# Performance work log

Measured on AMD Instinct MI355X. Metric: run time of the kernel, lower is better.

The kernel has to match this reference:

```python
import jax, jax.numpy as jnp
import numpy as np
from functools import partial

B, S, T = 32, 64, 64
VS, VT = 32000, 32000
E, H = 256, 512            # embed_dim, encoder hidden per direction
DH = 2 * H                 # decoder hidden (= encoder_hidden_dim)
A = 128                    # attention_dim


def _p(key, shape, scale=0.05):
    return scale * jax.random.normal(key, shape, dtype=jnp.float32)


def setup_inputs() -> dict:
    key = jax.random.key(0)
    ks = jax.random.split(key, 32)
    inp = {
        'src': jax.random.randint(ks[0], (B, S), 0, VS),
        'tgt_input': jax.random.randint(ks[1], (B, T), 0, VT),
        # encoder
        'enc_emb': _p(ks[2], (VS, E)),
        'enc_Wih_f': _p(ks[3], (4 * H, E)), 'enc_Whh_f': _p(ks[4], (4 * H, H)),
        'enc_bih_f': _p(ks[5], (4 * H,)),  'enc_bhh_f': _p(ks[6], (4 * H,)),
        'enc_Wih_b': _p(ks[7], (4 * H, E)), 'enc_Whh_b': _p(ks[8], (4 * H, H)),
        'enc_bih_b': _p(ks[9], (4 * H,)),  'enc_bhh_b': _p(ks[10], (4 * H,)),
        # decoder
        'dec_emb': _p(ks[11], (VT, E)),
        'Wd': _p(ks[12], (A, DH)), 'bd': _p(ks[13], (A,)),
        'We': _p(ks[14], (A, DH)), 'be': _p(ks[15], (A,)),
        'v_att': _p(ks[16], (A,)), 'bv': _p(ks[17], ()),
        'dec_Wih': _p(ks[18], (4 * DH, E + DH)), 'dec_Whh': _p(ks[19], (4 * DH, DH)),
        'dec_bih': _p(ks[20], (4 * DH,)), 'dec_bhh': _p(ks[21], (4 * DH,)),
        'Wo': _p(ks[22], (VT, DH + DH)), 'bo': _p(ks[23], (VT,)),
    }
    return inp


def _lstm_cell(x, h, c, Wih, Whh, b):
    g = x @ Wih.T + h @ Whh.T + b
    i, f, gg, o = jnp.split(g, 4, axis=-1)  # PyTorch gate order: i,f,g,o
    i, f, o = jax.nn.sigmoid(i), jax.nn.sigmoid(f), jax.nn.sigmoid(o)
    c_new = f * c + i * jnp.tanh(gg)
    h_new = o * jnp.tanh(c_new)
    return h_new, c_new


def _lstm_scan(xs, Wih, Whh, b, reverse):
    # xs: [S,B,E] -> outputs [S,B,H] aligned with input positions, final (h,c)
    h0 = jnp.zeros((xs.shape[1], Whh.shape[1]), xs.dtype)
    def step(carry, x):
        h, c = carry
        h, c = _lstm_cell(x, h, c, Wih, Whh, b)
        return (h, c), h
    (hT, cT), hs = jax.lax.scan(step, (h0, h0), xs, reverse=reverse)
    return hs, hT, cT


def _forward(src, tgt_input, enc_emb,
             enc_Wih_f, enc_Whh_f, enc_bih_f, enc_bhh_f,
             enc_Wih_b, enc_Whh_b, enc_bih_b, enc_bhh_b,
             dec_emb, Wd, bd, We, be, v_att, bv,
             dec_Wih, dec_Whh, dec_bih, dec_bhh, Wo, bo):
    # ---- Encoder: bidirectional single-layer LSTM ----
    emb = enc_emb[src]                              # [B,S,E]
    xs = emb.transpose(1, 0, 2)                     # [S,B,E]
    hs_f, hT_f, cT_f = _lstm_scan(xs, enc_Wih_f, enc_Whh_f, enc_bih_f + enc_bhh_f, False)
    hs_b, hT_b, cT_b = _lstm_scan(xs, enc_Wih_b, enc_Whh_b, enc_bih_b + enc_bhh_b, True)
    enc_out = jnp.concatenate([hs_f, hs_b], axis=-1).transpose(1, 0, 2)  # [B,S,2H]
    h = jnp.concatenate([hT_f, hT_b], axis=-1)      # [B,DH]
    c = jnp.concatenate([cT_f, cT_b], axis=-1)

    # ---- Decoder with Bahdanau attention (full teacher forcing) ----
    enc_proj = enc_out @ We.T + be                  # [B,S,A] precomputed
    dec_b = dec_bih + dec_bhh
    tgt_emb = dec_emb[tgt_input].transpose(1, 0, 2)  # [T,B,E]

    def dec_step(carry, emb_t):
        h, c = carry
        dproj = h @ Wd.T + bd                       # [B,A]
        energy = jnp.tanh(dproj[:, None, :] + enc_proj)  # [B,S,A]
        scores = energy @ v_att + bv                # [B,S]
        w = jax.nn.softmax(scores, axis=1)
        ctx = jnp.einsum('bs,bsh->bh', w, enc_out)  # [B,DH]
        x = jnp.concatenate([emb_t, ctx], axis=-1)  # [B,E+DH]
        h_new, c_new = _lstm_cell(x, h, c, dec_Wih, dec_Whh, dec_b)
        logits = jnp.concatenate([h_new, ctx], axis=-1) @ Wo.T + bo  # [B,VT]
        return (h_new, c_new), logits

    _, logits = jax.lax.scan(dec_step, (h, c), tgt_emb)  # [T,B,VT]
    return logits.transpose(1, 0, 2)                     # [B,T,VT]


def reference(src, tgt_input, enc_emb,
              enc_Wih_f, enc_Whh_f, enc_bih_f, enc_bhh_f,
              enc_Wih_b, enc_Whh_b, enc_bih_b, enc_bhh_b,
              dec_emb, Wd, bd, We, be, v_att, bv,
              dec_Wih, dec_Whh, dec_bih, dec_bhh, Wo, bo):
    return _forward(src, tgt_input, enc_emb,
                    enc_Wih_f, enc_Whh_f, enc_bih_f, enc_bhh_f,
                    enc_Wih_b, enc_Whh_b, enc_bih_b, enc_bhh_b,
                    dec_emb, Wd, bd, We, be, v_att, bv,
                    dec_Wih, dec_Whh, dec_bih, dec_bhh, Wo, bo)
```

## Files before the change

### kernel.cpp

```cpp
#include <hip/hip_runtime.h>


using u16 = unsigned short;
using u32 = unsigned int;
using u64 = unsigned long long;
using f32x4 = __attribute__((ext_vector_type(4))) float;
using s16x8 = __attribute__((ext_vector_type(8))) short;
using u16x4 = __attribute__((ext_vector_type(4))) unsigned short;

__device__ __forceinline__ float sigm_(float x) { return 1.0f / (1.0f + expf(-x)); }
__device__ __forceinline__ float tanh_(float x) {
    float e = __expf(fminf(2.0f * x, 30.0f));
    return (e - 1.0f) / (e + 1.0f);
}

__device__ __forceinline__ u16 f2bf(float x) {
    u32 u = __float_as_uint(x);
    u += 0x7fffu + ((u >> 16) & 1u);
    return (u16)(u >> 16);
}
__device__ __forceinline__ u32 pk2(float a, float b) {
    return (u32)f2bf(a) | ((u32)f2bf(b) << 16);
}
__device__ __forceinline__ float bf2f(u16 v) {
    return __uint_as_float((u32)v << 16);
}

__device__ __forceinline__ void ast32(u32* p, u32 v) {
    __hip_atomic_store(p, v, __ATOMIC_RELAXED, __HIP_MEMORY_SCOPE_AGENT);
}

#define MFMA __builtin_amdgcn_mfma_f32_16x16x32_bf16

#define GLL(g, l) __builtin_amdgcn_global_load_lds( \
    (__attribute__((address_space(1))) void*)(g),   \
    (__attribute__((address_space(3))) void*)(l), 16, 0, 0)

__device__ __forceinline__ void gbar(int* cnt, int target) {
    asm volatile("s_waitcnt vmcnt(0) lgkmcnt(0)" ::: "memory");
    __syncthreads();
    if (threadIdx.x == 0) {
        __hip_atomic_fetch_add(cnt, 1, __ATOMIC_RELAXED, __HIP_MEMORY_SCOPE_AGENT);
        while (__hip_atomic_load(cnt, __ATOMIC_RELAXED, __HIP_MEMORY_SCOPE_AGENT) < target)
            __builtin_amdgcn_s_sleep(1);
    }
    __syncthreads();
}

__global__ __launch_bounds__(256) void k_zero(float* __restrict__ p, int n) {
    int i = blockIdx.x * 256 + threadIdx.x;
    if (i < n) p[i] = 0.0f;
}

__global__ __launch_bounds__(256) void k_cast_bf16(const float* __restrict__ in,
                                                   u16* __restrict__ outp, int n8) {
    int idx = blockIdx.x * 256 + threadIdx.x;
    if (idx >= n8) return;
    const f32x4* p = (const f32x4*)in + (size_t)idx * 2;
    f32x4 a = p[0], c = p[1];
    u32* o = (u32*)(outp + (size_t)idx * 8);
    o[0] = pk2(a.x, a.y); o[1] = pk2(a.z, a.w);
    o[2] = pk2(c.x, c.y); o[3] = pk2(c.z, c.w);
}

__global__ __launch_bounds__(256) void k_embed_bf(const int* __restrict__ tok,
                                                  const float* __restrict__ emb,
                                                  u16* __restrict__ outp) {
    int idx = blockIdx.x * 256 + threadIdx.x;
    int r = idx >> 6, e4 = idx & 63;
    int outer = r >> 5, b = r & 31;
    int tk = tok[b * 64 + outer];
    f32x4 v = ((const f32x4*)emb)[(size_t)tk * 64 + e4];
    u32* o = (u32*)(outp + (size_t)r * 256 + (e4 << 2));
    o[0] = pk2(v.x, v.y); o[1] = pk2(v.z, v.w);
}

__global__ __launch_bounds__(256) void k_prep_perm(
    const float* __restrict__ src, u16* __restrict__ dst,
    int J, int K4, int srcStride, int srcOff, int total)
{
    int idx = blockIdx.x * 256 + threadIdx.x;
    if (idx >= total) return;
    int n = idx / K4, kq = (idx - n * K4) << 2;
    int orig = (n & 3) * J + (n >> 2);
    f32x4 v = *(const f32x4*)(src + (size_t)orig * srcStride + srcOff + kq);
    u32* o = (u32*)(dst + (size_t)n * (K4 << 2) + kq);
    o[0] = pk2(v.x, v.y); o[1] = pk2(v.z, v.w);
}

__global__ __launch_bounds__(256) void k_prep_ws(
    const float* __restrict__ W, u16* __restrict__ dst)
{
    int idx = blockIdx.x * 256 + threadIdx.x;
    int n = idx >> 8, kp = idx & 255, k0 = kp << 1;
    int orig = (n & 3) * 512 + (n >> 2);
    const float* s = W + (size_t)orig * 512 + k0;
    int g = n >> 5, r = n & 31;
    int byteoff = (k0 << 1) ^ ((r & 7) << 4);
    *(u32*)((char*)dst + (size_t)g * 32768 + r * 1024 + byteoff) = pk2(s[0], s[1]);
}

__global__ __launch_bounds__(256) void k_prep_w2s(
    const float* __restrict__ Whh, const float* __restrict__ Wih, u16* __restrict__ dst)
{
    int idx = blockIdx.x * 256 + threadIdx.x;
    int n = idx >> 10, kp = idx & 1023, k0 = kp << 1;
    int orig = (n & 3) * 1024 + (n >> 2);
    const float* s = (k0 < 1024) ? (Whh + (size_t)orig * 1024 + k0)
                                 : (Wih + (size_t)orig * 1280 + 256 + (k0 - 1024));
    int g = n >> 5, r = n & 31;
    int byteoff = (k0 << 1) ^ ((r & 7) << 4);
    *(u32*)((char*)dst + (size_t)g * 131072 + r * 4096 + byteoff) = pk2(s[0], s[1]);
}

__global__ __launch_bounds__(256) void k_gemm_bf(
    const u16* __restrict__ A, const u16* __restrict__ B, int K,
    const float* __restrict__ b1, const float* __restrict__ b2, int biasJ,
    float* __restrict__ C, int ldc, int nM, int nN, int remapOut, int swz)
{
    __shared__ __align__(16) u16 As[128 * 32];
    __shared__ __align__(16) u16 Bs[128 * 32];
    int w = blockIdx.x;
    if (swz) { int cpx = (nM * nN) >> 3; w = (w & 7) * cpx + (w >> 3); }
    int bm = (w % nM) * 128, bn = (w / nM) * 128;
    int tid = threadIdx.x, wave = tid >> 6, lane = tid & 63;
    int wm = wave & 1, wn = wave >> 1;
    f32x4 acc[4][4] = {};

    int rA = wave * 32 + (lane >> 2);
    int cb2 = (lane & 3) * 16;
    const char* gA = (const char*)A + ((size_t)(bm + rA) * K) * 2 + cb2;
    const char* gB = (const char*)B + ((size_t)(bn + rA) * K) * 2 + cb2;
    size_t rowskip = (size_t)16 * K * 2;
    char* lA = (char*)As + wave * 2048;
    char* lB = (char*)Bs + wave * 2048;
    const u16* rdA = As + (wm * 64 + (lane & 15)) * 32 + (lane >> 4) * 8;
    const u16* rdB = Bs + (wn * 64 + (lane & 15)) * 32 + (lane >> 4) * 8;

    for (int k0 = 0; k0 < K; k0 += 32) {
        size_t kb = (size_t)k0 * 2;
        GLL(gA + kb, lA); GLL(gA + kb + rowskip, lA + 1024);
        GLL(gB + kb, lB); GLL(gB + kb + rowskip, lB + 1024);
        __syncthreads();
        s16x8 af[4], bfv[4];
#pragma unroll
        for (int m2 = 0; m2 < 4; ++m2) af[m2] = *(const s16x8*)(rdA + m2 * 512);
#pragma unroll
        for (int n2 = 0; n2 < 4; ++n2) bfv[n2] = *(const s16x8*)(rdB + n2 * 512);
#pragma unroll
        for (int m2 = 0; m2 < 4; ++m2)
#pragma unroll
            for (int n2 = 0; n2 < 4; ++n2)
                acc[m2][n2] = MFMA(af[m2], bfv[n2], acc[m2][n2], 0, 0, 0);
        __syncthreads();
    }

    int rbase = bm + wm * 64 + ((lane >> 4) << 2);
    int cbase = bn + wn * 64 + (lane & 15);
#pragma unroll
    for (int n2 = 0; n2 < 4; ++n2) {
        int col = cbase + n2 * 16;
        int bcol = biasJ ? ((col & 3) * biasJ + (col >> 2)) : col;
        float bias = (b1 ? b1[bcol] : 0.0f) + (b2 ? b2[bcol] : 0.0f);
#pragma unroll
        for (int m2 = 0; m2 < 4; ++m2) {
            f32x4 v = acc[m2][n2];
#pragma unroll
            for (int jj = 0; jj < 4; ++jj) {
                int row = rbase + m2 * 16 + jj;
                int orow = remapOut ? ((row & 31) * 64 + (row >> 5)) : row;
                C[(size_t)orow * ldc + col] = v[jj] + bias;
            }
        }
    }
}

__global__ __launch_bounds__(256, 1) void k_enc_persist(
    const u16* __restrict__ Wsf, const u16* __restrict__ Wsb,
    const float* __restrict__ Gfp, const float* __restrict__ Gbp,
    u16* __restrict__ henc,
    float* __restrict__ cfb,
    u16* __restrict__ encbf,
    int* __restrict__ bar)
{
    __shared__ __align__(16) char smem[50176];
    int tid = threadIdx.x, lane = tid & 63, q = tid >> 6;
    int dir = blockIdx.x >> 6, g = blockIdx.x & 63;
    const char* wsrc = (const char*)(dir ? Wsb : Wsf) + (size_t)g * 32768;
#pragma unroll
    for (int it = 0; it < 8; ++it)
        GLL(wsrc + it * 4096 + tid * 16, smem + it * 4096 + tid * 16);
    __syncthreads();

    float* sacc = (float*)(smem + 32768);
    u16* hst = (u16*)(smem + 49664);
    const float* Gp = dir ? Gbp : Gfp;
    float* cB = cfb + dir * 16384;
    int lr = lane & 15, lk = (lane >> 4) << 3;
    int bb = tid & 31, jl = tid >> 5;
    int n0 = g * 32, j = g * 8 + jl;
    int bi = 0;

    for (int s = 0; s < 64; ++s) {
        const u16* hA = henc + (size_t)s * 32768 + dir * 16384;
        s16x8 afr[8];
#pragma unroll
        for (int it = 0; it < 4; ++it) {
            int ke = q * 128 + it * 32 + lk;
            afr[2 * it]     = *(const s16x8*)(hA + lr * 512 + ke);
            afr[2 * it + 1] = *(const s16x8*)(hA + (lr + 16) * 512 + ke);
        }
        f32x4 acc00 = {}, acc01 = {}, acc10 = {}, acc11 = {};
#pragma unroll
        for (int it = 0; it < 4; ++it) {
            int ke = q * 128 + it * 32 + lk;
            int kb = ke << 1;
            s16x8 b0 = *(const s16x8*)(smem + lr * 1024 + (kb ^ ((lr & 7) << 4)));
            int r1 = lr + 16;
            s16x8 b1 = *(const s16x8*)(smem + r1 * 1024 + (kb ^ ((r1 & 7) << 4)));
            acc00 = MFMA(afr[2 * it], b0, acc00, 0, 0, 0);
            acc01 = MFMA(afr[2 * it], b1, acc01, 0, 0, 0);
            acc10 = MFMA(afr[2 * it + 1], b0, acc10, 0, 0, 0);
            acc11 = MFMA(afr[2 * it + 1], b1, acc11, 0, 0, 0);
        }
        int rw = (lane >> 4) << 2;
#pragma unroll
        for (int rr = 0; rr < 4; ++rr) {
            sacc[q * 1056 + (rw + rr) * 33 + lr]        = acc00[rr];
            sacc[q * 1056 + (rw + rr) * 33 + 16 + lr]   = acc01[rr];
            sacc[q * 1056 + (16 + rw + rr) * 33 + lr]      = acc10[rr];
            sacc[q * 1056 + (16 + rw + rr) * 33 + 16 + lr] = acc11[rr];
        }
        __syncthreads();
        {
            int t = dir ? (63 - s) : s;
            int c4 = jl << 2;
            float gi = 0, gf = 0, gg = 0, go2 = 0;
#pragma unroll
            for (int q2 = 0; q2 < 4; ++q2) {
                const float* sp = sacc + q2 * 1056 + bb * 33 + c4;
                gi += sp[0]; gf += sp[1]; gg += sp[2]; go2 += sp[3];
            }
            f32x4 p4 = *(const f32x4*)(Gp + ((size_t)(t * 32 + bb)) * 2048 + n0 + c4);
            gi += p4.x; gf += p4.y; gg += p4.z; go2 += p4.w;
            float* cp = cB + bb * 512 + j;
            float cn = sigm_(gf) * cp[0] + sigm_(gi) * tanhf(gg);
            cp[0] = cn;
            float h = sigm_(go2) * tanhf(cn);
            u16 h16 = f2bf(h);
            encbf[((size_t)(bb * 64 + t)) * 1024 + dir * 512 + j] = h16;
            hst[bb * 8 + jl] = h16;
        }
        __syncthreads();
        if (tid < 128) {
            int bb2 = tid >> 2, p2 = tid & 3;
            u32 wv = (u32)hst[bb2 * 8 + 2 * p2] | ((u32)hst[bb2 * 8 + 2 * p2 + 1] << 16);
            ast32((u32*)(henc + (size_t)(s + 1) * 32768 + dir * 16384) + bb2 * 256 + g * 4 + p2, wv);
        }
        gbar(bar, (++bi) * 128);
    }
}

__global__ __launch_bounds__(256) void k_dec_init(
    const u16* __restrict__ henc, const float* __restrict__ cfb,
    u16* __restrict__ hcarr, float* __restrict__ cd)
{
    int idx = blockIdx.x * 256 + threadIdx.x;
    int b = idx >> 10, j = idx & 1023;
    int dir = (j >> 9), jj = j & 511;
    hcarr[b * 2048 + j] = henc[(size_t)64 * 32768 + dir * 16384 + b * 512 + jj];
    cd[b * 1024 + j] = cfb[dir * 16384 + b * 512 + jj];
}

__global__ __launch_bounds__(256, 1) void k_dec_persist(
    const u16* __restrict__ W2s, const u16* __restrict__ encbf,
    const float* __restrict__ Prep,
    const u16* __restrict__ Wd_bf, const float* __restrict__ bd,
    const float* __restrict__ eproj, const float* __restrict__ v_att,
    const float* __restrict__ bv,
    u16* __restrict__ hcarr, float* __restrict__ cd, u16* __restrict__ Abf,
    int* __restrict__ bar)
{
    __shared__ __align__(16) char smem[148480];
    int blk = blockIdx.x, tid = threadIdx.x, lane = tid & 63, q = tid >> 6;
    bool isgate = blk < 128;
    {
        const char* src = isgate ? ((const char*)W2s + (size_t)blk * 131072)
                                 : ((const char*)encbf + (size_t)(blk - 128) * 131072);
#pragma unroll
        for (int it = 0; it < 32; ++it)
            GLL(src + it * 4096 + tid * 16, smem + it * 4096 + tid * 16);
    }
    __syncthreads();

    float* sacc = (float*)(smem + 131072);
    u16* hst    = (u16*)(smem + 147968);
    float* hsh  = (float*)(smem + 131072);
    float* red  = (float*)(smem + 135168);
    float* dp   = (float*)(smem + 136192);
    float* sc   = (float*)(smem + 136704);

    int lr = lane & 15, lk = (lane >> 4) << 3;
    int bb = tid & 31, jl = tid >> 5;
    int n0 = blk * 32, j = blk * 8 + jl;
    int b = blk - 128;
    int bi = 0;

    for (int t = 0; t < 64; ++t) {
        const u16* hcT = hcarr + (size_t)t * 65536;
        f32x4 acc00 = {}, acc01 = {}, acc10 = {}, acc11 = {};
        f32x4 p4;
        if (isgate) {
            p4 = *(const f32x4*)(Prep + ((size_t)(t * 32 + bb)) * 4096 + n0 + (jl << 2));
            s16x8 afr[16];
#pragma unroll
            for (int it = 0; it < 8; ++it) {
                int ke = q * 256 + it * 32 + lk;
                afr[2 * it]     = *(const s16x8*)(hcT + lr * 2048 + ke);
                afr[2 * it + 1] = *(const s16x8*)(hcT + (lr + 16) * 2048 + ke);
            }
#pragma unroll
            for (int it = 0; it < 8; ++it) {
                int ke = q * 256 + it * 32 + lk;
                int kb = ke << 1;
                s16x8 b0 = *(const s16x8*)(smem + lr * 4096 + (kb ^ ((lr & 7) << 4)));
                int r1 = lr + 16;
                s16x8 b1 = *(const s16x8*)(smem + r1 * 4096 + (kb ^ ((r1 & 7) << 4)));
                acc00 = MFMA(afr[2 * it], b0, acc00, 0, 0, 0);
                acc01 = MFMA(afr[2 * it], b1, acc01, 0, 0, 0);
                acc10 = MFMA(afr[2 * it + 1], b0, acc10, 0, 0, 0);
                acc11 = MFMA(afr[2 * it + 1], b1, acc11, 0, 0, 0);
            }
        } else {
            {
                u16x4 hv = *(const u16x4*)(hcT + b * 2048 + (tid << 2));
                hsh[(tid << 2) + 0] = bf2f(hv.x);
                hsh[(tid << 2) + 1] = bf2f(hv.y);
                hsh[(tid << 2) + 2] = bf2f(hv.z);
                hsh[(tid << 2) + 3] = bf2f(hv.w);
            }
            __syncthreads();
            {
                int a = tid & 127, half = tid >> 7;
                const u16* wr = Wd_bf + ((size_t)a << 10) + (half << 9);
                const float* hh = hsh + (half << 9);
                float s0 = 0, s1 = 0, s2 = 0, s3 = 0;
#pragma unroll 4
                for (int k = 0; k < 512; k += 32) {
                    s16x8 w0 = *(const s16x8*)(wr + k);
                    s16x8 w1 = *(const s16x8*)(wr + k + 8);
                    s16x8 w2 = *(const s16x8*)(wr + k + 16);
                    s16x8 w3 = *(const s16x8*)(wr + k + 24);
#pragma unroll
                    for (int e = 0; e < 8; ++e) {
                        s0 += bf2f((u16)w0[e]) * hh[k + e];
                        s1 += bf2f((u16)w1[e]) * hh[k + 8 + e];
                        s2 += bf2f((u16)w2[e]) * hh[k + 16 + e];
                        s3 += bf2f((u16)w3[e]) * hh[k + 24 + e];
                    }
                }
                red[tid] = (s0 + s1) + (s2 + s3);
            }
            __syncthreads();
            if (tid < 128) dp[tid] = red[tid] + red[tid + 128] + bd[tid];
            __syncthreads();
            {
                int si = tid >> 2, qq = tid & 3;
                const float* ep = eproj + ((size_t)(b * 64 + si)) * 128 + qq * 32;
                float s = 0.0f;
#pragma unroll 8
                for (int a2 = 0; a2 < 32; ++a2)
                    s += v_att[qq * 32 + a2] * tanh_(dp[qq * 32 + a2] + ep[a2]);
                red[tid] = s;
            }
            __syncthreads();
            if (tid < 64) {
                float x = red[tid * 4] + red[tid * 4 + 1] + red[tid * 4 + 2] + red[tid * 4 + 3] + bv[0];
                float mx = x;
#pragma unroll
                for (int off = 32; off; off >>= 1) mx = fmaxf(mx, __shfl_xor(mx, off));
                float e = __expf(x - mx), ss = e;
#pragma unroll
                for (int off = 32; off; off >>= 1) ss += __shfl_xor(ss, off);
                sc[tid] = e / ss;
            }
            __syncthreads();
            {
                const u16* eL = (const u16*)smem;
                int c0i = tid << 2;
                float c0 = 0, c1 = 0, c2 = 0, c3 = 0;
                for (int s2 = 0; s2 < 64; ++s2) {
                    float wgt = sc[s2];
                    u16x4 rp = *(const u16x4*)(eL + s2 * 1024 + c0i);
                    c0 += wgt * bf2f(rp.x); c1 += wgt * bf2f(rp.y);
                    c2 += wgt * bf2f(rp.z); c3 += wgt * bf2f(rp.w);
                }
                u32 w0 = pk2(c0, c1), w1 = pk2(c2, c3);
                u32* hw = (u32*)hcT + b * 1024 + 512 + (tid << 1);
                ast32(hw, w0); ast32(hw + 1, w1);
                u32* aw = (u32*)(Abf + ((size_t)(t * 32 + b)) * 2048 + 1024 + c0i);
                aw[0] = w0; aw[1] = w1;
            }
        }
        gbar(bar, (++bi) * 160);
        if (isgate) {
            s16x8 afr[16];
#pragma unroll
            for (int it = 0; it < 8; ++it) {
                int ke = 1024 + q * 256 + it * 32 + lk;
                afr[2 * it]     = *(const s16x8*)(hcT + lr * 2048 + ke);
                afr[2 * it + 1] = *(const s16x8*)(hcT + (lr + 16) * 2048 + ke);
            }
#pragma unroll
            for (int it = 0; it < 8; ++it) {
                int ke = 1024 + q * 256 + it * 32 + lk;
                int kb = ke << 1;
                s16x8 b0 = *(const s16x8*)(smem + lr * 4096 + (kb ^ ((lr & 7) << 4)));
                int r1 = lr + 16;
                s16x8 b1 = *(const s16x8*)(smem + r1 * 4096 + (kb ^ ((r1 & 7) << 4)));
                acc00 = MFMA(afr[2 * it], b0, acc00, 0, 0, 0);
                acc01 = MFMA(afr[2 * it], b1, acc01, 0, 0, 0);
                acc10 = MFMA(afr[2 * it + 1], b0, acc10, 0, 0, 0);
                acc11 = MFMA(afr[2 * it + 1], b1, acc11, 0, 0, 0);
            }
            int rw = (lane >> 4) << 2;
#pragma unroll
            for (int rr = 0; rr < 4; ++rr) {
                sacc[q * 1056 + (rw + rr) * 33 + lr]        = acc00[rr];
                sacc[q * 1056 + (rw + rr) * 33 + 16 + lr]   = acc01[rr];
                sacc[q * 1056 + (16 + rw + rr) * 33 + lr]      = acc10[rr];
                sacc[q * 1056 + (16 + rw + rr) * 33 + 16 + lr] = acc11[rr];
            }
            __syncthreads();
            {
                int c4 = jl << 2;
                float gi = 0, gf = 0, gg = 0, go2 = 0;
#pragma unroll
                for (int q2 = 0; q2 < 4; ++q2) {
                    const float* sp = sacc + q2 * 1056 + bb * 33 + c4;
                    gi += sp[0]; gf += sp[1]; gg += sp[2]; go2 += sp[3];
                }
                gi += p4.x; gf += p4.y; gg += p4.z; go2 += p4.w;
                int ci = bb * 1024 + j;
                float cn = sigm_(gf) * cd[ci] + sigm_(gi) * tanhf(gg);
                cd[ci] = cn;
                float h = sigm_(go2) * tanhf(cn);
                u16 h16 = f2bf(h);
                Abf[((size_t)(t * 32 + bb)) * 2048 + j] = h16;
                hst[bb * 8 + jl] = h16;
            }
            __syncthreads();
            if (tid < 128) {
                int bb2 = tid >> 2, p2 = tid & 3;
                u32 wv = (u32)hst[bb2 * 8 + 2 * p2] | ((u32)hst[bb2 * 8 + 2 * p2 + 1] << 16);
                ast32((u32*)(hcarr + (size_t)(t + 1) * 65536) + bb2 * 1024 + blk * 4 + p2, wv);
            }
        }
        gbar(bar, (++bi) * 160);
    }
}

extern "C" void kernel_launch(void* const* d_in, const int* in_sizes, int n_in,
                              void* d_out, int out_size, void* d_ws, size_t ws_size,
                              hipStream_t stream)
{
    (void)in_sizes; (void)n_in; (void)out_size; (void)ws_size;
    const int*   src     = (const int*)d_in[0];
    const int*   tgt     = (const int*)d_in[1];
    const float* enc_emb = (const float*)d_in[2];
    const float* eWih_f  = (const float*)d_in[3];
    const float* eWhh_f  = (const float*)d_in[4];
    const float* ebih_f  = (const float*)d_in[5];
    const float* ebhh_f  = (const float*)d_in[6];
    const float* eWih_b  = (const float*)d_in[7];
    const float* eWhh_b  = (const float*)d_in[8];
    const float* ebih_b  = (const float*)d_in[9];
    const float* ebhh_b  = (const float*)d_in[10];
    const float* dec_emb = (const float*)d_in[11];
    const float* Wd      = (const float*)d_in[12];
    const float* bd      = (const float*)d_in[13];
    const float* We      = (const float*)d_in[14];
    const float* be      = (const float*)d_in[15];
    const float* v_att   = (const float*)d_in[16];
    const float* bv      = (const float*)d_in[17];
    const float* dWih    = (const float*)d_in[18];
    const float* dWhh    = (const float*)d_in[19];
    const float* dbih    = (const float*)d_in[20];
    const float* dbhh    = (const float*)d_in[21];
    const float* Wo      = (const float*)d_in[22];
    const float* bo      = (const float*)d_in[23];
    float* out = (float*)d_out;

    char* wp = (char*)d_ws;
    auto alloc = [&](size_t nbytes) -> void* {
        void* p = (void*)wp;
        wp += (nbytes + 255) & ~(size_t)255;
        return p;
    };
    u16*   Xe_bf = (u16*)alloc(2048u * 256 * 2);
    u16*   Ed_bf = (u16*)alloc(2048u * 256 * 2);
    float* Gf_p  = (float*)alloc(2048u * 2048 * 4);
    float* Gb_p  = (float*)alloc(2048u * 2048 * 4);
    float* Pre_p = (float*)alloc(2048u * 4096 * 4);
    float* zr    = (float*)alloc(131584u);
    float* cfb   = zr;
    int*   cnts  = (int*)((char*)zr + 131072);
    u16*   henc  = (u16*)alloc(65u * 32768 * 2);
    u16*   hcarr = (u16*)alloc(65u * 65536 * 2);
    u16*   encbf = (u16*)alloc(2048u * 1024 * 2);
    float* eproj = (float*)alloc(2048u * 128 * 4);
    float* cd    = (float*)alloc(32768u * 4);
    u16*   Abf   = (u16*)alloc(2048u * 2048 * 2);
    u16*   Wbf   = (u16*)alloc(32000u * 2048 * 2);
    u16*   W2s   = (u16*)alloc(4096u * 2048 * 2);
    u16*   Wsf   = (u16*)alloc(2048u * 512 * 2);
    u16*   Wsb   = (u16*)alloc(2048u * 512 * 2);
    u16*   Wembf = (u16*)alloc(2048u * 256 * 2);
    u16*   Wembb = (u16*)alloc(2048u * 256 * 2);
    u16*   Wembd = (u16*)alloc(4096u * 256 * 2);
    u16*   We_bf = (u16*)alloc(128u * 1024 * 2);
    u16*   Wd_bf = (u16*)alloc(128u * 1024 * 2);

    k_zero<<<129, 256, 0, stream>>>(zr, 32896);
    k_zero<<<64, 256, 0, stream>>>((float*)henc, 16384);

    k_cast_bf16<<<32000, 256, 0, stream>>>(Wo, Wbf, 8192000);
    k_cast_bf16<<<64, 256, 0, stream>>>(We, We_bf, 16384);
    k_cast_bf16<<<64, 256, 0, stream>>>(Wd, Wd_bf, 16384);
    k_prep_perm<<<512, 256, 0, stream>>>(eWih_f, Wembf, 512, 64, 256, 0, 131072);
    k_prep_perm<<<512, 256, 0, stream>>>(eWih_b, Wembb, 512, 64, 256, 0, 131072);
    k_prep_perm<<<1024, 256, 0, stream>>>(dWih, Wembd, 1024, 64, 1280, 0, 262144);
    k_prep_ws<<<2048, 256, 0, stream>>>(eWhh_f, Wsf);
    k_prep_ws<<<2048, 256, 0, stream>>>(eWhh_b, Wsb);
    k_prep_w2s<<<16384, 256, 0, stream>>>(dWhh, dWih, W2s);

    k_embed_bf<<<512, 256, 0, stream>>>(src, enc_emb, Xe_bf);
    k_embed_bf<<<512, 256, 0, stream>>>(tgt, dec_emb, Ed_bf);

    k_gemm_bf<<<256, 256, 0, stream>>>(Xe_bf, Wembf, 256, ebih_f, ebhh_f, 512,
                                       Gf_p, 2048, 16, 16, 0, 1);
    k_gemm_bf<<<256, 256, 0, stream>>>(Xe_bf, Wembb, 256, ebih_b, ebhh_b, 512,
                                       Gb_p, 2048, 16, 16, 0, 1);
    k_gemm_bf<<<512, 256, 0, stream>>>(Ed_bf, Wembd, 256, dbih, dbhh, 1024,
                                       Pre_p, 4096, 16, 32, 0, 1);

    k_enc_persist<<<128, 256, 0, stream>>>(Wsf, Wsb, Gf_p, Gb_p, henc, cfb, encbf, cnts);

    k_gemm_bf<<<16, 256, 0, stream>>>(encbf, We_bf, 1024, be, nullptr, 0,
                                      eproj, 128, 16, 1, 0, 1);
    k_dec_init<<<128, 256, 0, stream>>>(henc, cfb, hcarr, cd);

    k_dec_persist<<<160, 256, 0, stream>>>(W2s, encbf, Pre_p, Wd_bf, bd, eproj,
                                           v_att, bv, hcarr, cd, Abf, cnts + 64);

    k_gemm_bf<<<4000, 256, 0, stream>>>(Abf, Wbf, 2048, bo, nullptr, 0,
                                        out, 32000, 16, 250, 1, 1);
}
```

Measured before the change: 2.375 ms.

## Precompute encoder-context projection and use per-step hierarchical flag barriers in decoder

```diff
diff --git a/kernel.cpp b/kernel.cpp
--- a/kernel.cpp
+++ b/kernel.cpp
@@ -36,15 +36,24 @@
     (__attribute__((address_space(1))) void*)(g),   \
     (__attribute__((address_space(3))) void*)(l), 16, 0, 0)
 
-__device__ __forceinline__ void gbar(int* cnt, int target) {
+__device__ __forceinline__ void poll8(const int* go8) {
+    if (threadIdx.x < 8) {
+        const int* p = go8 + threadIdx.x * 16;
+        while (__hip_atomic_load(p, __ATOMIC_RELAXED, __HIP_MEMORY_SCOPE_AGENT) == 0)
+            __builtin_amdgcn_s_sleep(1);
+    }
+    __syncthreads();
+    asm volatile("" ::: "memory");
+}
+__device__ __forceinline__ void arrive8(int* cnt8, int* go8, int line, int perline) {
     asm volatile("s_waitcnt vmcnt(0) lgkmcnt(0)" ::: "memory");
     __syncthreads();
     if (threadIdx.x == 0) {
-        __hip_atomic_fetch_add(cnt, 1, __ATOMIC_RELAXED, __HIP_MEMORY_SCOPE_AGENT);
-        while (__hip_atomic_load(cnt, __ATOMIC_RELAXED, __HIP_MEMORY_SCOPE_AGENT) < target)
-            __builtin_amdgcn_s_sleep(1);
-    }
-    __syncthreads();
+        int old = __hip_atomic_fetch_add(cnt8 + line * 16, 1, __ATOMIC_RELAXED,
+                                         __HIP_MEMORY_SCOPE_AGENT);
+        if (old == perline - 1)
+            __hip_atomic_store(go8 + line * 16, 1, __ATOMIC_RELAXED, __HIP_MEMORY_SCOPE_AGENT);
+    }
 }
 
 __global__ __launch_bounds__(256) void k_zero(float* __restrict__ p, int n) {
@@ -100,23 +109,23 @@
     *(u32*)((char*)dst + (size_t)g * 32768 + r * 1024 + byteoff) = pk2(s[0], s[1]);
 }
 
-__global__ __launch_bounds__(256) void k_prep_w2s(
-    const float* __restrict__ Whh, const float* __restrict__ Wih, u16* __restrict__ dst)
+__global__ __launch_bounds__(256) void k_prep_whhs(
+    const float* __restrict__ Whh, u16* __restrict__ dst)
 {
     int idx = blockIdx.x * 256 + threadIdx.x;
-    int n = idx >> 10, kp = idx & 1023, k0 = kp << 1;
+    int n = idx >> 9, kp = idx & 511, k0 = kp << 1;
     int orig = (n & 3) * 1024 + (n >> 2);
-    const float* s = (k0 < 1024) ? (Whh + (size_t)orig * 1024 + k0)
-                                 : (Wih + (size_t)orig * 1280 + 256 + (k0 - 1024));
-    int g = n >> 5, r = n & 31;
+    const float* s = Whh + (size_t)orig * 1024 + k0;
+    int g = n >> 6, r = n & 63;
     int byteoff = (k0 << 1) ^ ((r & 7) << 4);
-    *(u32*)((char*)dst + (size_t)g * 131072 + r * 4096 + byteoff) = pk2(s[0], s[1]);
+    *(u32*)((char*)dst + (size_t)g * 131072 + r * 2048 + byteoff) = pk2(s[0], s[1]);
 }
 
 __global__ __launch_bounds__(256) void k_gemm_bf(
     const u16* __restrict__ A, const u16* __restrict__ B, int K,
     const float* __restrict__ b1, const float* __restrict__ b2, int biasJ,
-    float* __restrict__ C, int ldc, int nM, int nN, int remapOut, int swz)
+    float* __restrict__ C, int ldc, int nM, int nN, int remapOut, int swz,
+    u16* __restrict__ outT)
 {
     __shared__ __align__(16) u16 As[128 * 32];
     __shared__ __align__(16) u16 Bs[128 * 32];
@@ -157,6 +166,20 @@
 
     int rbase = bm + wm * 64 + ((lane >> 4) << 2);
     int cbase = bn + wn * 64 + (lane & 15);
+    if (outT) {
+#pragma unroll
+        for (int n2 = 0; n2 < 4; ++n2) {
+            int col = cbase + n2 * 16;
+#pragma unroll
+            for (int m2 = 0; m2 < 4; ++m2) {
+                f32x4 v = acc[m2][n2];
+                int row = rbase + m2 * 16;
+                u32* o = (u32*)(outT + (size_t)col * 2048 + row);
+                o[0] = pk2(v[0], v[1]); o[1] = pk2(v[2], v[3]);
+            }
+        }
+        return;
+    }
 #pragma unroll
     for (int n2 = 0; n2 < 4; ++n2) {
         int col = cbase + n2 * 16;
@@ -181,7 +204,7 @@
     u16* __restrict__ henc,
     float* __restrict__ cfb,
     u16* __restrict__ encbf,
-    int* __restrict__ bar)
+    int* __restrict__ cnt8, int* __restrict__ go8)
 {
     __shared__ __align__(16) char smem[50176];
     int tid = threadIdx.x, lane = tid & 63, q = tid >> 6;
@@ -199,9 +222,11 @@
     int lr = lane & 15, lk = (lane >> 4) << 3;
     int bb = tid & 31, jl = tid >> 5;
     int n0 = g * 32, j = g * 8 + jl;
-    int bi = 0;
 
     for (int s = 0; s < 64; ++s) {
+        if (s) poll8(go8 + s * 128);
+        int t = dir ? (63 - s) : s;
+        f32x4 p4 = *(const f32x4*)(Gp + ((size_t)(t * 32 + bb)) * 2048 + n0 + (jl << 2));
         const u16* hA = henc + (size_t)s * 32768 + dir * 16384;
         s16x8 afr[8];
 #pragma unroll
@@ -233,7 +258,6 @@
         }
         __syncthreads();
         {
-            int t = dir ? (63 - s) : s;
             int c4 = jl << 2;
             float gi = 0, gf = 0, gg = 0, go2 = 0;
 #pragma unroll
@@ -241,7 +265,6 @@
                 const float* sp = sacc + q2 * 1056 + bb * 33 + c4;
                 gi += sp[0]; gf += sp[1]; gg += sp[2]; go2 += sp[3];
             }
-            f32x4 p4 = *(const f32x4*)(Gp + ((size_t)(t * 32 + bb)) * 2048 + n0 + c4);
             gi += p4.x; gf += p4.y; gg += p4.z; go2 += p4.w;
             float* cp = cB + bb * 512 + j;
             float cn = sigm_(gf) * cp[0] + sigm_(gi) * tanhf(gg);
@@ -257,7 +280,7 @@
             u32 wv = (u32)hst[bb2 * 8 + 2 * p2] | ((u32)hst[bb2 * 8 + 2 * p2 + 1] << 16);
             ast32((u32*)(henc + (size_t)(s + 1) * 32768 + dir * 16384) + bb2 * 256 + g * 4 + p2, wv);
         }
-        gbar(bar, (++bi) * 128);
+        arrive8(cnt8 + (s + 1) * 128, go8 + (s + 1) * 128, blockIdx.x & 7, 16);
     }
 }
 
@@ -268,25 +291,27 @@
     int idx = blockIdx.x * 256 + threadIdx.x;
     int b = idx >> 10, j = idx & 1023;
     int dir = (j >> 9), jj = j & 511;
-    hcarr[b * 2048 + j] = henc[(size_t)64 * 32768 + dir * 16384 + b * 512 + jj];
+    hcarr[b * 1024 + j] = henc[(size_t)64 * 32768 + dir * 16384 + b * 512 + jj];
     cd[b * 1024 + j] = cfb[dir * 16384 + b * 512 + jj];
 }
 
 __global__ __launch_bounds__(256, 1) void k_dec_persist(
-    const u16* __restrict__ W2s, const u16* __restrict__ encbf,
-    const float* __restrict__ Prep,
+    const u16* __restrict__ Whhs, const u16* __restrict__ encbf,
+    const float* __restrict__ Prep, const u16* __restrict__ ectxT,
     const u16* __restrict__ Wd_bf, const float* __restrict__ bd,
     const float* __restrict__ eproj, const float* __restrict__ v_att,
     const float* __restrict__ bv,
     u16* __restrict__ hcarr, float* __restrict__ cd, u16* __restrict__ Abf,
-    int* __restrict__ bar)
-{
-    __shared__ __align__(16) char smem[148480];
-    int blk = blockIdx.x, tid = threadIdx.x, lane = tid & 63, q = tid >> 6;
-    bool isgate = blk < 128;
+    float* __restrict__ wbuf,
+    int* __restrict__ hCnt8, int* __restrict__ goH8,
+    int* __restrict__ wCnt8, int* __restrict__ goW8)
+{
+    __shared__ __align__(16) char smem[148736];
+    int blk = blockIdx.x, tid = threadIdx.x, lane = tid & 63, w = tid >> 6;
+    bool isgate = blk < 64;
     {
-        const char* src = isgate ? ((const char*)W2s + (size_t)blk * 131072)
-                                 : ((const char*)encbf + (size_t)(blk - 128) * 131072);
+        const char* src = isgate ? ((const char*)Whhs + (size_t)blk * 131072)
+                                 : ((const char*)encbf + (size_t)(blk - 64) * 131072);
 #pragma unroll
         for (int it = 0; it < 32; ++it)
             GLL(src + it * 4096 + tid * 16, smem + it * 4096 + tid * 16);
@@ -294,46 +319,107 @@
     __syncthreads();
 
     float* sacc = (float*)(smem + 131072);
-    u16* hst    = (u16*)(smem + 147968);
+    float* wsh  = (float*)(smem + 139520);
+    u16*   hst  = (u16*)(smem + 147712);
     float* hsh  = (float*)(smem + 131072);
     float* red  = (float*)(smem + 135168);
     float* dp   = (float*)(smem + 136192);
     float* sc   = (float*)(smem + 136704);
 
     int lr = lane & 15, lk = (lane >> 4) << 3;
-    int bb = tid & 31, jl = tid >> 5;
-    int n0 = blk * 32, j = blk * 8 + jl;
-    int b = blk - 128;
-    int bi = 0;
+    int b = blk - 64;
+    int n0 = blk * 64, j0 = blk * 16;
 
     for (int t = 0; t < 64; ++t) {
-        const u16* hcT = hcarr + (size_t)t * 65536;
-        f32x4 acc00 = {}, acc01 = {}, acc10 = {}, acc11 = {};
-        f32x4 p4;
+        if (t) poll8(goH8 + t * 128);
+        const u16* hT = hcarr + (size_t)t * 32768;
         if (isgate) {
-            p4 = *(const f32x4*)(Prep + ((size_t)(t * 32 + bb)) * 4096 + n0 + (jl << 2));
-            s16x8 afr[16];
-#pragma unroll
-            for (int it = 0; it < 8; ++it) {
-                int ke = q * 256 + it * 32 + lk;
-                afr[2 * it]     = *(const s16x8*)(hcT + lr * 2048 + ke);
-                afr[2 * it + 1] = *(const s16x8*)(hcT + (lr + 16) * 2048 + ke);
-            }
-#pragma unroll
-            for (int it = 0; it < 8; ++it) {
-                int ke = q * 256 + it * 32 + lk;
-                int kb = ke << 1;
-                s16x8 b0 = *(const s16x8*)(smem + lr * 4096 + (kb ^ ((lr & 7) << 4)));
-                int r1 = lr + 16;
-                s16x8 b1 = *(const s16x8*)(smem + r1 * 4096 + (kb ^ ((r1 & 7) << 4)));
-                acc00 = MFMA(afr[2 * it], b0, acc00, 0, 0, 0);
-                acc01 = MFMA(afr[2 * it], b1, acc01, 0, 0, 0);
-                acc10 = MFMA(afr[2 * it + 1], b0, acc10, 0, 0, 0);
-                acc11 = MFMA(afr[2 * it + 1], b1, acc11, 0, 0, 0);
-            }
+            int jl = tid >> 5, bb = tid & 31;
+            f32x4 pA = *(const f32x4*)(Prep + ((size_t)(t * 32 + bb)) * 4096 + n0 + (jl << 2));
+            f32x4 pB = *(const f32x4*)(Prep + ((size_t)(t * 32 + bb)) * 4096 + n0 + ((jl + 8) << 2));
+            f32x4 acc0 = {}, acc1 = {};
+            int rB = w * 16 + lr;
+            int xw = (rB & 7) << 4;
+#pragma unroll
+            for (int ch = 0; ch < 4; ++ch) {
+                s16x8 afr[16];
+#pragma unroll
+                for (int it = 0; it < 8; ++it) {
+                    int ke = ch * 256 + it * 32 + lk;
+                    afr[2 * it]     = *(const s16x8*)(hT + lr * 1024 + ke);
+                    afr[2 * it + 1] = *(const s16x8*)(hT + (lr + 16) * 1024 + ke);
+                }
+#pragma unroll
+                for (int it = 0; it < 8; ++it) {
+                    int ke = ch * 256 + it * 32 + lk;
+                    s16x8 b0 = *(const s16x8*)(smem + rB * 2048 + ((ke << 1) ^ xw));
+                    acc0 = MFMA(afr[2 * it], b0, acc0, 0, 0, 0);
+                    acc1 = MFMA(afr[2 * it + 1], b0, acc1, 0, 0, 0);
+                }
+            }
+            int rw = (lane >> 4) << 2;
+#pragma unroll
+            for (int rr = 0; rr < 4; ++rr) {
+                sacc[(rw + rr) * 66 + w * 16 + lr]      = acc0[rr];
+                sacc[(16 + rw + rr) * 66 + w * 16 + lr] = acc1[rr];
+            }
+            __syncthreads();
+            poll8(goW8 + t * 128);
+            {
+                const f32x4* wsrc = (const f32x4*)(wbuf + (size_t)t * 2048);
+                f32x4 w0 = wsrc[tid * 2], w1 = wsrc[tid * 2 + 1];
+                ((f32x4*)wsh)[tid * 2] = w0; ((f32x4*)wsh)[tid * 2 + 1] = w1;
+            }
+            __syncthreads();
+            {
+                int nl = tid >> 2, bbase = (tid & 3) * 8;
+                const u16* ebase = ectxT + (size_t)(n0 + nl) * 2048;
+#pragma unroll
+                for (int i = 0; i < 8; ++i) {
+                    int b2 = bbase + i;
+                    const u16* er = ebase + b2 * 64;
+                    const float* wr = wsh + b2 * 64;
+                    float s = 0.0f;
+#pragma unroll
+                    for (int ss = 0; ss < 64; ss += 8) {
+                        s16x8 ev = *(const s16x8*)(er + ss);
+                        f32x4 wv0 = *(const f32x4*)(wr + ss);
+                        f32x4 wv1 = *(const f32x4*)(wr + ss + 4);
+                        s += bf2f((u16)ev[0]) * wv0.x + bf2f((u16)ev[1]) * wv0.y
+                           + bf2f((u16)ev[2]) * wv0.z + bf2f((u16)ev[3]) * wv0.w
+                           + bf2f((u16)ev[4]) * wv1.x + bf2f((u16)ev[5]) * wv1.y
+                           + bf2f((u16)ev[6]) * wv1.z + bf2f((u16)ev[7]) * wv1.w;
+                    }
+                    sacc[b2 * 66 + nl] += s;
+                }
+            }
+            __syncthreads();
+            {
+#pragma unroll
+                for (int half = 0; half < 2; ++half) {
+                    int jloc = jl + half * 8;
+                    const float* sp = sacc + bb * 66 + (jloc << 2);
+                    f32x4 p4 = half ? pB : pA;
+                    float gi = sp[0] + p4.x, gf = sp[1] + p4.y;
+                    float gg = sp[2] + p4.z, go2 = sp[3] + p4.w;
+                    int ci = bb * 1024 + j0 + jloc;
+                    float cn = sigm_(gf) * cd[ci] + sigm_(gi) * tanhf(gg);
+                    cd[ci] = cn;
+                    float h = sigm_(go2) * tanhf(cn);
+                    hst[bb * 16 + jloc] = f2bf(h);
+                }
+            }
+            __syncthreads();
+            {
+                int b2 = tid >> 3, wd = tid & 7;
+                u32 wv = (u32)hst[b2 * 16 + 2 * wd] | ((u32)hst[b2 * 16 + 2 * wd + 1] << 16);
+                ast32((u32*)(hcarr + (size_t)(t + 1) * 32768) + (b2 * 1024 + j0) / 2 + wd, wv);
+                *((u32*)(Abf + ((size_t)(t * 32 + b2)) * 2048 + j0) + wd) = wv;
+            }
+            arrive8(hCnt8 + (t + 1) * 128, goH8 + (t + 1) * 128, blk & 7, 8);
         } else {
             {
-                u16x4 hv = *(const u16x4*)(hcT + b * 2048 + (tid << 2));
+                u16x4 hv = *(const u16x4*)(hT + b * 1024 + (tid << 2));
                 hsh[(tid << 2) + 0] = bf2f(hv.x);
                 hsh[(tid << 2) + 1] = bf2f(hv.y);
                 hsh[(tid << 2) + 2] = bf2f(hv.z);
@@ -382,9 +468,11 @@
                 float e = __expf(x - mx), ss = e;
 #pragma unroll
                 for (int off = 32; off; off >>= 1) ss += __shfl_xor(ss, off);
-                sc[tid] = e / ss;
-            }
-            __syncthreads();
+                float wgt = e / ss;
+                sc[tid] = wgt;
+                ast32((u32*)(wbuf + (size_t)t * 2048 + b * 64) + tid, __float_as_uint(wgt));
+            }
+            arrive8(wCnt8 + t * 128, goW8 + t * 128, blk & 7, 4);
             {
                 const u16* eL = (const u16*)smem;
                 int c0i = tid << 2;
@@ -395,68 +483,10 @@
                     c0 += wgt * bf2f(rp.x); c1 += wgt * bf2f(rp.y);
                     c2 += wgt * bf2f(rp.z); c3 += wgt * bf2f(rp.w);
                 }
-                u32 w0 = pk2(c0, c1), w1 = pk2(c2, c3);
-                u32* hw = (u32*)hcT + b * 1024 + 512 + (tid << 1);
-                ast32(hw, w0); ast32(hw + 1, w1);
                 u32* aw = (u32*)(Abf + ((size_t)(t * 32 + b)) * 2048 + 1024 + c0i);
-                aw[0] = w0; aw[1] = w1;
-            }
-        }
-        gbar(bar, (++bi) * 160);
-        if (isgate) {
-            s16x8 afr[16];
-#pragma unroll
-            for (int it = 0; it < 8; ++it) {
-                int ke = 1024 + q * 256 + it * 32 + lk;
-                afr[2 * it]     = *(const s16x8*)(hcT + lr * 2048 + ke);
-                afr[2 * it + 1] = *(const s16x8*)(hcT + (lr + 16) * 2048 + ke);
-            }
-#pragma unroll
-            for (int it = 0; it < 8; ++it) {
-                int ke = 1024 + q * 256 + it * 32 + lk;
-                int kb = ke << 1;
-                s16x8 b0 = *(const s16x8*)(smem + lr * 4096 + (kb ^ ((lr & 7) << 4)));
-                int r1 = lr + 16;
-                s16x8 b1 = *(const s16x8*)(smem + r1 * 4096 + (kb ^ ((r1 & 7) << 4)));
-                acc00 = MFMA(afr[2 * it], b0, acc00, 0, 0, 0);
-                acc01 = MFMA(afr[2 * it], b1, acc01, 0, 0, 0);
-                acc10 = MFMA(afr[2 * it + 1], b0, acc10, 0, 0, 0);
-                acc11 = MFMA(afr[2 * it + 1], b1, acc11, 0, 0, 0);
-            }
-            int rw = (lane >> 4) << 2;
-#pragma unroll
-            for (int rr = 0; rr < 4; ++rr) {
-                sacc[q * 1056 + (rw + rr) * 33 + lr]        = acc00[rr];
-                sacc[q * 1056 + (rw + rr) * 33 + 16 + lr]   = acc01[rr];
-                sacc[q * 1056 + (16 + rw + rr) * 33 + lr]      = acc10[rr];
-                sacc[q * 1056 + (16 + rw + rr) * 33 + 16 + lr] = acc11[rr];
-            }
-            __syncthreads();
-            {
-                int c4 = jl << 2;
-                float gi = 0, gf = 0, gg = 0, go2 = 0;
-#pragma unroll
-                for (int q2 = 0; q2 < 4; ++q2) {
-                    const float* sp = sacc + q2 * 1056 + bb * 33 + c4;
-                    gi += sp[0]; gf += sp[1]; gg += sp[2]; go2 += sp[3];
-                }
-                gi += p4.x; gf += p4.y; gg += p4.z; go2 += p4.w;
-                int ci = bb * 1024 + j;
-                float cn = sigm_(gf) * cd[ci] + sigm_(gi) * tanhf(gg);
-                cd[ci] = cn;
-                float h = sigm_(go2) * tanhf(cn);
-                u16 h16 = f2bf(h);
-                Abf[((size_t)(t * 32 + bb)) * 2048 + j] = h16;
-                hst[bb * 8 + jl] = h16;
-            }
-            __syncthreads();
-            if (tid < 128) {
-                int bb2 = tid >> 2, p2 = tid & 3;
-                u32 wv = (u32)hst[bb2 * 8 + 2 * p2] | ((u32)hst[bb2 * 8 + 2 * p2 + 1] << 16);
-                ast32((u32*)(hcarr + (size_t)(t + 1) * 65536) + bb2 * 1024 + blk * 4 + p2, wv);
-            }
-        }
-        gbar(bar, (++bi) * 160);
+                aw[0] = pk2(c0, c1); aw[1] = pk2(c2, c3);
+            }
+        }
     }
 }
 
@@ -497,31 +527,40 @@
         wp += (nbytes + 255) & ~(size_t)255;
         return p;
     };
-    u16*   Xe_bf = (u16*)alloc(2048u * 256 * 2);
-    u16*   Ed_bf = (u16*)alloc(2048u * 256 * 2);
-    float* Gf_p  = (float*)alloc(2048u * 2048 * 4);
-    float* Gb_p  = (float*)alloc(2048u * 2048 * 4);
-    float* Pre_p = (float*)alloc(2048u * 4096 * 4);
-    float* zr    = (float*)alloc(131584u);
-    float* cfb   = zr;
-    int*   cnts  = (int*)((char*)zr + 131072);
-    u16*   henc  = (u16*)alloc(65u * 32768 * 2);
-    u16*   hcarr = (u16*)alloc(65u * 65536 * 2);
-    u16*   encbf = (u16*)alloc(2048u * 1024 * 2);
-    float* eproj = (float*)alloc(2048u * 128 * 4);
-    float* cd    = (float*)alloc(32768u * 4);
-    u16*   Abf   = (u16*)alloc(2048u * 2048 * 2);
-    u16*   Wbf   = (u16*)alloc(32000u * 2048 * 2);
-    u16*   W2s   = (u16*)alloc(4096u * 2048 * 2);
-    u16*   Wsf   = (u16*)alloc(2048u * 512 * 2);
-    u16*   Wsb   = (u16*)alloc(2048u * 512 * 2);
-    u16*   Wembf = (u16*)alloc(2048u * 256 * 2);
-    u16*   Wembb = (u16*)alloc(2048u * 256 * 2);
-    u16*   Wembd = (u16*)alloc(4096u * 256 * 2);
-    u16*   We_bf = (u16*)alloc(128u * 1024 * 2);
-    u16*   Wd_bf = (u16*)alloc(128u * 1024 * 2);
-
-    k_zero<<<129, 256, 0, stream>>>(zr, 32896);
+    u16*   Xe_bf  = (u16*)alloc(2048u * 256 * 2);
+    u16*   Ed_bf  = (u16*)alloc(2048u * 256 * 2);
+    float* Gf_p   = (float*)alloc(2048u * 2048 * 4);
+    float* Gb_p   = (float*)alloc(2048u * 2048 * 4);
+    float* Pre_p  = (float*)alloc(2048u * 4096 * 4);
+    float* zr     = (float*)alloc(329728u);
+    float* cfb    = zr;
+    char*  sy     = (char*)zr + 131072;
+    int*   cntE8  = (int*)(sy);
+    int*   goE8   = (int*)(sy + 33280);
+    int*   hCnt8  = (int*)(sy + 66560);
+    int*   goH8   = (int*)(sy + 99840);
+    int*   wCnt8  = (int*)(sy + 133120);
+    int*   goW8   = (int*)(sy + 165888);
+    u16*   henc   = (u16*)alloc(65u * 32768 * 2);
+    u16*   hcarr  = (u16*)alloc(65u * 32768 * 2);
+    u16*   encbf  = (u16*)alloc(2048u * 1024 * 2);
+    float* eproj  = (float*)alloc(2048u * 128 * 4);
+    float* cd     = (float*)alloc(32768u * 4);
+    float* wbuf   = (float*)alloc(64u * 2048 * 4);
+    u16*   Abf    = (u16*)alloc(2048u * 2048 * 2);
+    u16*   Wbf    = (u16*)alloc(32000u * 2048 * 2);
+    u16*   Whhs   = (u16*)alloc(4096u * 1024 * 2);
+    u16*   Wctx_p = (u16*)alloc(4096u * 1024 * 2);
+    u16*   ectxT  = (u16*)alloc(4096u * 2048 * 2);
+    u16*   Wsf    = (u16*)alloc(2048u * 512 * 2);
+    u16*   Wsb    = (u16*)alloc(2048u * 512 * 2);
+    u16*   Wembf  = (u16*)alloc(2048u * 256 * 2);
+    u16*   Wembb  = (u16*)alloc(2048u * 256 * 2);
+    u16*   Wembd  = (u16*)alloc(4096u * 256 * 2);
+    u16*   We_bf  = (u16*)alloc(128u * 1024 * 2);
+    u16*   Wd_bf  = (u16*)alloc(128u * 1024 * 2);
+
+    k_zero<<<322, 256, 0, stream>>>(zr, 82432);
     k_zero<<<64, 256, 0, stream>>>((float*)henc, 16384);
 
     k_cast_bf16<<<32000, 256, 0, stream>>>(Wo, Wbf, 8192000);
@@ -530,29 +569,34 @@
     k_prep_perm<<<512, 256, 0, stream>>>(eWih_f, Wembf, 512, 64, 256, 0, 131072);
     k_prep_perm<<<512, 256, 0, stream>>>(eWih_b, Wembb, 512, 64, 256, 0, 131072);
     k_prep_perm<<<1024, 256, 0, stream>>>(dWih, Wembd, 1024, 64, 1280, 0, 262144);
+    k_prep_perm<<<4096, 256, 0, stream>>>(dWih, Wctx_p, 1024, 256, 1280, 256, 1048576);
     k_prep_ws<<<2048, 256, 0, stream>>>(eWhh_f, Wsf);
     k_prep_ws<<<2048, 256, 0, stream>>>(eWhh_b, Wsb);
-    k_prep_w2s<<<16384, 256, 0, stream>>>(dWhh, dWih, W2s);
+    k_prep_whhs<<<8192, 256, 0, stream>>>(dWhh, Whhs);
 
     k_embed_bf<<<512, 256, 0, stream>>>(src, enc_emb, Xe_bf);
     k_embed_bf<<<512, 256, 0, stream>>>(tgt, dec_emb, Ed_bf);
 
     k_gemm_bf<<<256, 256, 0, stream>>>(Xe_bf, Wembf, 256, ebih_f, ebhh_f, 512,
-                                       Gf_p, 2048, 16, 16, 0, 1);
+                                       Gf_p, 2048, 16, 16, 0, 1, nullptr);
     k_gemm_bf<<<256, 256, 0, stream>>>(Xe_bf, Wembb, 256, ebih_b, ebhh_b, 512,
-                                       Gb_p, 2048, 16, 16, 0, 1);
+                                       Gb_p, 2048, 16, 16, 0, 1, nullptr);
     k_gemm_bf<<<512, 256, 0, stream>>>(Ed_bf, Wembd, 256, dbih, dbhh, 1024,
-                                       Pre_p, 4096, 16, 32, 0, 1);
-
-    k_enc_persist<<<128, 256, 0, stream>>>(Wsf, Wsb, Gf_p, Gb_p, henc, cfb, encbf, cnts);
+                                       Pre_p, 4096, 16, 32, 0, 1, nullptr);
+
+    k_enc_persist<<<128, 256, 0, stream>>>(Wsf, Wsb, Gf_p, Gb_p, henc, cfb, encbf,
+                                           cntE8, goE8);
 
     k_gemm_bf<<<16, 256, 0, stream>>>(encbf, We_bf, 1024, be, nullptr, 0,
-                                      eproj, 128, 16, 1, 0, 1);
+                                      eproj, 128, 16, 1, 0, 1, nullptr);
+    k_gemm_bf<<<512, 256, 0, stream>>>(encbf, Wctx_p, 1024, nullptr, nullptr, 0,
+                                       nullptr, 0, 16, 32, 0, 1, ectxT);
     k_dec_init<<<128, 256, 0, stream>>>(henc, cfb, hcarr, cd);
 
-    k_dec_persist<<<160, 256, 0, stream>>>(W2s, encbf, Pre_p, Wd_bf, bd, eproj,
-                                           v_att, bv, hcarr, cd, Abf, cnts + 64);
+    k_dec_persist<<<96, 256, 0, stream>>>(Whhs, encbf, Pre_p, ectxT, Wd_bf, bd, eproj,
+                                          v_att, bv, hcarr, cd, Abf, wbuf,
+                                          hCnt8, goH8, wCnt8, goW8);
 
     k_gemm_bf<<<4000, 256, 0, stream>>>(Abf, Wbf, 2048, bo, nullptr, 0,
-                                        out, 32000, 16, 250, 1, 1);
-}
+                                        out, 32000, 16, 250, 1, 1, nullptr);
+}
```

Result: slower. 2.475 ms (+4.2%).
